# Optimization experiments

Measured on AMD Instinct MI355X. Metric: run time of the kernel, lower is better.

The kernel has to match this reference:

```python
import jax, jax.numpy as jnp
import numpy as np

NUM_CLASSES = 2
THRESH = 0.5        # overlap_thresh
NEGPOS = 3          # neg:pos ratio
VAR = (0.1, 0.2)    # cfg['variance']
B, P, O = 64, 32768, 50


def point_form(p):
    # center-size [cx,cy,w,h] -> corner [xmin,ymin,xmax,ymax]
    return jnp.concatenate([p[:, :2] - p[:, 2:] * 0.5, p[:, :2] + p[:, 2:] * 0.5], axis=1)


def iou(a, b):
    # a [O,4], b [P,4] corner form -> [O,P]
    lt = jnp.maximum(a[:, None, :2], b[None, :, :2])
    rb = jnp.minimum(a[:, None, 2:], b[None, :, 2:])
    wh = jnp.clip(rb - lt, 0.0, None)
    inter = wh[..., 0] * wh[..., 1]
    area_a = ((a[:, 2] - a[:, 0]) * (a[:, 3] - a[:, 1]))[:, None]
    area_b = ((b[:, 2] - b[:, 0]) * (b[:, 3] - b[:, 1]))[None, :]
    return inter / (area_a + area_b - inter)


def encode(matched, priors_cs):
    g_cxcy = ((matched[:, :2] + matched[:, 2:]) * 0.5 - priors_cs[:, :2]) / (VAR[0] * priors_cs[:, 2:])
    g_wh = jnp.log((matched[:, 2:] - matched[:, :2]) / priors_cs[:, 2:]) / VAR[1]
    return jnp.concatenate([g_cxcy, g_wh], axis=1)


def match_one(truths, labels, priors_cs, priors_pt):
    ovl = iou(truths, priors_pt)                # [O,P]
    best_prior_idx = jnp.argmax(ovl, axis=1)    # [O] best prior per GT
    best_truth_ovl = jnp.max(ovl, axis=0)       # [P]
    best_truth_idx = jnp.argmax(ovl, axis=0)    # [P]
    best_truth_ovl = best_truth_ovl.at[best_prior_idx].set(2.0)
    best_truth_idx = best_truth_idx.at[best_prior_idx].set(jnp.arange(truths.shape[0]))
    matched = truths[best_truth_idx]            # [P,4]
    conf = jnp.where(best_truth_ovl < THRESH, 0, labels[best_truth_idx])
    return encode(matched, priors_cs), conf


def reference(arm_loc, arm_conf, odm_loc, odm_conf, priors, targets):
    loc_data, conf_data = arm_loc, arm_conf    # use_ARM=False -> ARM branch
    num, num_priors = loc_data.shape[0], loc_data.shape[1]
    truths = targets[..., :4]
    labels = (targets[..., 4] >= 0).astype(jnp.int32)   # num_classes == 2 binarization
    priors_pt = point_form(priors)
    loc_t, conf_t = jax.vmap(lambda t, l: match_one(t, l, priors, priors_pt))(truths, labels)
    loc_t = jax.lax.stop_gradient(loc_t)
    conf_t = jax.lax.stop_gradient(conf_t)
    pos = conf_t > 0                             # [B,P]
    # localization: smooth L1, summed over positives
    d = loc_data - loc_t
    ad = jnp.abs(d)
    sl1 = jnp.where(ad < 1.0, 0.5 * d * d, ad - 0.5)
    loss_l = jnp.sum(sl1 * pos[..., None].astype(loc_data.dtype))
    # per-prior conf loss for hard negative mining
    lse = jax.nn.logsumexp(conf_data, axis=-1)   # [B,P]
    picked = jnp.take_along_axis(conf_data, conf_t[..., None], axis=-1)[..., 0]
    lc = lse - picked                            # NLL per prior
    lc_mine = jnp.where(pos, 0.0, lc)            # zero positives before ranking
    order = jnp.argsort(-lc_mine, axis=1)        # descending sort
    rank = jnp.argsort(order, axis=1)            # rank of each prior
    num_pos = jnp.sum(pos, axis=1, keepdims=True)            # [B,1]
    num_neg = jnp.minimum(NEGPOS * num_pos, num_priors - 1)
    neg = rank < num_neg
    sel = (pos | neg).astype(conf_data.dtype)
    loss_c = jnp.sum(lc * sel)
    N = jnp.sum(num_pos).astype(loc_data.dtype)
    return loss_l / N, loss_c / N


def setup_inputs():
    key = jax.random.key(0)
    ks = jax.random.split(key, 8)
    arm_loc = jax.random.normal(ks[0], (B, P, 4), jnp.float32)
    arm_conf = jax.random.normal(ks[1], (B, P, NUM_CLASSES), jnp.float32)
    odm_loc = jax.random.normal(ks[2], (B, P, 4), jnp.float32)
    odm_conf = jax.random.normal(ks[3], (B, P, NUM_CLASSES), jnp.float32)
    # priors in center-size form
    p_cxcy = jax.random.uniform(ks[4], (P, 2), jnp.float32, 0.05, 0.95)
    p_wh = jax.random.uniform(ks[5], (P, 2), jnp.float32, 0.05, 0.5)
    priors = jnp.concatenate([p_cxcy, p_wh], axis=1)
    # GT boxes in corner form with valid extents, labels >= 0
    t_cxcy = jax.random.uniform(ks[6], (B, O, 2), jnp.float32, 0.2, 0.8)
    t_wh = jax.random.uniform(ks[7], (B, O, 2), jnp.float32, 0.05, 0.3)
    boxes = jnp.concatenate([t_cxcy - t_wh * 0.5, t_cxcy + t_wh * 0.5], axis=-1)
    targets = jnp.concatenate([boxes, jnp.ones((B, O, 1), jnp.float32)], axis=-1)
    return {"arm_loc": arm_loc, "arm_conf": arm_conf, "odm_loc": odm_loc,
            "odm_conf": odm_conf, "priors": priors, "targets": targets}
```

## Files before the change

### kernel.cpp

```cpp
#include <hip/hip_runtime.h>
#include <cstdint>

#pragma clang fp contract(off)

#define BB 64
#define PP 32768
#define OO 50
#define THRESH_F 0.5f
#define VAR0 0.1f
#define VAR1 0.2f
#define NEGPOS_I 3
#define SS 32
#define T1 4
#define NB0 2048
#define NB12 1024

typedef unsigned long long u64;

__global__ void k_zero(float4* __restrict__ dst, int n4) {
    int i = blockIdx.x * blockDim.x + threadIdx.x;
    if (i < n4) dst[i] = make_float4(0.f, 0.f, 0.f, 0.f);
}

#define DPP_MAX(x, ctrl, rmask)                                              \
    {                                                                        \
        int _o = __float_as_int(x);                                          \
        x = fmaxf(x, __int_as_float(__builtin_amdgcn_update_dpp(             \
                _o, _o, (ctrl), (rmask), 0xf, false)));                      \
    }

__device__ __forceinline__ float sl1enc(const float* __restrict__ tb,
                                        float4 pr, float4 ld) {
    float gx = ((tb[0] + tb[2]) * 0.5f - pr.x) / (VAR0 * pr.z);
    float gy = ((tb[1] + tb[3]) * 0.5f - pr.y) / (VAR0 * pr.w);
    float gw = logf((tb[2] - tb[0]) / pr.z) / VAR1;
    float gh = logf((tb[3] - tb[1]) / pr.w) / VAR1;
    float g[4] = {gx, gy, gw, gh};
    float l[4] = {ld.x, ld.y, ld.z, ld.w};
    float s = 0.f;
    for (int q = 0; q < 4; ++q) {
        float d = l[q] - g[q];
        float ad = fabsf(d);
        s += (ad < 1.0f) ? 0.5f * d * d : ad - 0.5f;
    }
    return s;
}

__global__ void __launch_bounds__(256, 8)
k_ml(const float* __restrict__ priors, const float* __restrict__ targets,
     const float* __restrict__ arm_loc, const float* __restrict__ arm_conf,
     float* __restrict__ lcm, unsigned char* __restrict__ bpi,
     u64* __restrict__ bpm,
     float* __restrict__ pll, float* __restrict__ pplc, int* __restrict__ pnp,
     int* __restrict__ Hc0, float* __restrict__ Hs0) {
    __shared__ float tr4[OO * 4];
    __shared__ float trA[OO];
    __shared__ int   trL[OO];
    __shared__ int   hc[NB0];
    __shared__ float hs[NB0];
    int b = blockIdx.y, tid = threadIdx.x;
    for (int i = tid; i < OO * 4; i += 256)
        tr4[i] = targets[(size_t)(b * OO + (i >> 2)) * 5 + (i & 3)];
    if (tid < OO)
        trL[tid] = (targets[(size_t)(b * OO + tid) * 5 + 4] >= 0.0f) ? 1 : 0;
    for (int i = tid; i < NB0; i += 256) { hc[i] = 0; hs[i] = 0.f; }
    __syncthreads();
    if (tid < OO)
        trA[tid] = (tr4[tid*4+2] - tr4[tid*4]) * (tr4[tid*4+3] - tr4[tid*4+1]);
    __syncthreads();

    int p0 = blockIdx.x * (256 * T1) + tid * T1;
    float bx0[T1], by0[T1], bx1[T1], by1[T1], aB[T1];
#pragma unroll
    for (int j = 0; j < T1; ++j) {
        float4 pr = ((const float4*)priors)[p0 + j];
        bx0[j] = pr.x - pr.z * 0.5f; by0[j] = pr.y - pr.w * 0.5f;
        bx1[j] = pr.x + pr.z * 0.5f; by1[j] = pr.y + pr.w * 0.5f;
        aB[j] = (bx1[j] - bx0[j]) * (by1[j] - by0[j]);
    }
    float rbv[T1]; int rbi[T1];
#pragma unroll
    for (int j = 0; j < T1; ++j) { rbv[j] = -1.0f; rbi[j] = 0; }

    for (int t = 0; t < OO; ++t) {
        float t0 = tr4[t*4], t1v = tr4[t*4+1], t2 = tr4[t*4+2], t3 = tr4[t*4+3];
        float aA = trA[t];
        float cbv = -1.0f; int cbp = 0;
#pragma unroll
        for (int j = 0; j < T1; ++j) {
            float ltx = fmaxf(t0, bx0[j]), lty = fmaxf(t1v, by0[j]);
            float rbx = fminf(t2, bx1[j]), rby = fminf(t3, by1[j]);
            float wx = fmaxf(rbx - ltx, 0.f), wy = fmaxf(rby - lty, 0.f);
            float inter = wx * wy;
            float v = inter / (aA + aB[j] - inter);
            if (v > rbv[j]) { rbv[j] = v; rbi[j] = t; }
            if (v > cbv) { cbv = v; cbp = p0 + j; }
        }
        float x = cbv;
        DPP_MAX(x, 0x111, 0xf);
        DPP_MAX(x, 0x112, 0xf);
        DPP_MAX(x, 0x114, 0xf);
        DPP_MAX(x, 0x118, 0xf);
        DPP_MAX(x, 0x142, 0xa);
        DPP_MAX(x, 0x143, 0xc);
        float mv = __int_as_float(__builtin_amdgcn_readlane(__float_as_int(x), 63));
        unsigned long long msk = __ballot(cbv == mv);
        int lane = (int)__ffsll((long long)msk) - 1;
        int pwin = __builtin_amdgcn_readlane(cbp, lane);
        if ((tid & 63) == 0) {
            u64 pk = ((u64)__float_as_uint(mv) << 32) | (unsigned)(PP - pwin);
            atomicMax(&bpm[b * OO + t], pk);
        }
    }

    size_t bp = (size_t)b * PP + p0;
    float4 ca = ((const float4*)arm_conf)[bp >> 1];
    float4 cb = ((const float4*)arm_conf)[(bp >> 1) + 1];
    float cs[8] = {ca.x, ca.y, ca.z, ca.w, cb.x, cb.y, cb.z, cb.w};

    float ll = 0.0f, plc = 0.0f; int np = 0;
    float outv[4]; unsigned pbyte = 0;
#pragma unroll
    for (int c = 0; c < 4; ++c) {
        int ti = rbi[c]; float ov = rbv[c];
        int conf = (ov < THRESH_F) ? 0 : trL[ti];
        float c0 = cs[c*2], c1 = cs[c*2+1];
        float m = fmaxf(c0, c1);
        float lse = logf(expf(c0 - m) + expf(c1 - m)) + m;
        bool pos = conf > 0;
        float lc = lse - (pos ? c1 : c0);
        outv[c] = pos ? 0.0f : lc;
        pbyte |= (unsigned)((pos ? 0x80u : 0u) | (unsigned)ti) << (8 * c);
        unsigned u = __float_as_uint(outv[c]);
        atomicAdd(&hc[u >> 20], 1);
        atomicAdd(&hs[u >> 20], outv[c]);
        if (pos) {
            np++; plc += lc;
            float4 pr = ((const float4*)priors)[p0 + c];
            float4 ld = ((const float4*)arm_loc)[bp + c];
            ll += sl1enc(&tr4[ti * 4], pr, ld);
        }
    }
    ((float4*)lcm)[bp >> 2] = make_float4(outv[0], outv[1], outv[2], outv[3]);
    ((unsigned*)bpi)[bp >> 2] = pbyte;

    __syncthreads();
    for (int i = tid; i < NB0; i += 256) {
        int cv = hc[i];
        if (cv) {
            atomicAdd(&Hc0[b * NB0 + i], cv);
            atomicAdd(&Hs0[b * NB0 + i], hs[i]);
        }
    }
    __syncthreads();
    float* s1 = (float*)hc;
    int*   s3 = hc + 256;
    float* s2 = hs;
    s1[tid] = ll; s2[tid] = plc; s3[tid] = np;
    __syncthreads();
    for (int st = 128; st > 0; st >>= 1) {
        if (tid < st) { s1[tid] += s1[tid+st]; s2[tid] += s2[tid+st]; s3[tid] += s3[tid+st]; }
        __syncthreads();
    }
    if (tid == 0) {
        pll[blockIdx.x * BB + b] = s1[0];
        pplc[blockIdx.x * BB + b] = s2[0];
        pnp[blockIdx.x * BB + b] = s3[0];
    }
}

__global__ void k_fix(const u64* __restrict__ bpm, const float* __restrict__ targets,
                      const float* __restrict__ arm_loc, const float* __restrict__ arm_conf,
                      const float* __restrict__ priors, const unsigned char* __restrict__ bpi,
                      float* __restrict__ lcm,
                      float* __restrict__ pll, float* __restrict__ pplc,
                      int* __restrict__ pnp, int* __restrict__ npb,
                      int* __restrict__ Hc0, float* __restrict__ Hs0) {
    int b = blockIdx.x, j = threadIdx.x;
    int p = -1;
    if (j < OO) p = PP - (int)(unsigned)(bpm[b * OO + j] & 0xFFFFFFFFull);
    bool w = (j < OO);
    for (int jj = 1; jj < OO; ++jj) {
        int pj = __shfl(p, jj, 64);
        if (jj > j && pj == p) w = false;
    }
    float dll = 0.f, dplc = 0.f; int dnp = 0;
    if (w) {
        size_t bp = (size_t)b * PP + p;
        unsigned char ob = bpi[bp];
        bool old_pos = (ob & 0x80u) != 0;
        int old_ti = ob & 63;
        float2 cf = ((const float2*)arm_conf)[bp];
        float c0 = cf.x, c1 = cf.y;
        float m = fmaxf(c0, c1);
        float lse = logf(expf(c0 - m) + expf(c1 - m)) + m;
        const float* tbj = &targets[(size_t)(b * OO + j) * 5];
        bool new_pos = (tbj[4] >= 0.0f);
        float old_lcm = lcm[bp];
        float new_lcm = new_pos ? 0.0f : (lse - c0);
        unsigned uo = __float_as_uint(old_lcm), un = __float_as_uint(new_lcm);
        if (uo != un) {
            atomicAdd(&Hc0[b * NB0 + (uo >> 20)], -1);
            atomicAdd(&Hs0[b * NB0 + (uo >> 20)], -old_lcm);
            atomicAdd(&Hc0[b * NB0 + (un >> 20)], 1);
            atomicAdd(&Hs0[b * NB0 + (un >> 20)], new_lcm);
            lcm[bp] = new_lcm;
        }
        float4 pr = ((const float4*)priors)[p];
        float4 ld = ((const float4*)arm_loc)[bp];
        if (old_pos) {
            dnp -= 1; dplc -= (lse - c1);
            dll -= sl1enc(&targets[(size_t)(b * OO + old_ti) * 5], pr, ld);
        }
        if (new_pos) {
            dnp += 1; dplc += (lse - c1);
            dll += sl1enc(tbj, pr, ld);
        }
    }
    int myp = (j < SS) ? pnp[j * BB + b] : 0;
    for (int s = 32; s >= 1; s >>= 1) {
        dll += __shfl_down(dll, s, 64);
        dplc += __shfl_down(dplc, s, 64);
        dnp += __shfl_down(dnp, s, 64);
        myp += __shfl_down(myp, s, 64);
    }
    if (j == 0) {
        pll[b] += dll;
        pplc[b] += dplc;
        pnp[b] += dnp;
        npb[b] = myp + dnp;
    }
}

__global__ void __launch_bounds__(256)
k_sel(const float* __restrict__ lcm, const int* __restrict__ npb,
      int* __restrict__ Hc0, float* __restrict__ Hs0,
      float* __restrict__ ssum, int* __restrict__ srem, unsigned* __restrict__ stb) {
    __shared__ int hc[NB12]; __shared__ float hs[NB12];
    __shared__ int sc[256]; __shared__ float sf[256];
    __shared__ int s_chunk, s_r; __shared__ float s_S; __shared__ unsigned s_pref;
    int b = blockIdx.x, tid = threadIdx.x;

    {
        const int* hcg = Hc0 + b * NB0; const float* hsg = Hs0 + b * NB0;
        int c = 0; float f = 0.f; int base = tid * 8;
        for (int i = 0; i < 8; ++i) { c += hcg[base + i]; f += hsg[base + i]; }
        sc[tid] = c; sf[tid] = f;
        if (tid == 0) {
            int k = NEGPOS_I * npb[b]; if (k > PP - 1) k = PP - 1;
            s_r = k; s_S = 0.f;
        }
        __syncthreads();
        for (int off = 1; off < 256; off <<= 1) {
            int cv = (tid + off < 256) ? sc[tid + off] : 0;
            float fv = (tid + off < 256) ? sf[tid + off] : 0.f;
            __syncthreads(); sc[tid] += cv; sf[tid] += fv; __syncthreads();
        }
        int r = s_r;
        int nxt = (tid == 255) ? 0 : sc[tid + 1];
        if (sc[tid] >= r && nxt < r) s_chunk = tid;
        __syncthreads();
        if (tid == 0) {
            int ch = s_chunk;
            int r2 = r - ((ch == 255) ? 0 : sc[ch + 1]);
            float S2 = s_S + ((ch == 255) ? 0.f : sf[ch + 1]);
            int binSel = ch * 8;
            for (int i = 7; i >= 0; --i) {
                int bin = ch * 8 + i; int cbn = hcg[bin];
                if (r2 <= cbn) { binSel = bin; break; }
                r2 -= cbn; S2 += hsg[bin];
            }
            s_pref = (unsigned)binSel; s_r = r2; s_S = S2;
        }
        __syncthreads();
    }
    {
        for (int i = tid; i < NB12; i += 256) { hc[i] = 0; hs[i] = 0.f; }
        __syncthreads();
        unsigned pref = s_pref;
        const float4* v4 = (const float4*)(lcm + (size_t)b * PP);
        for (int it = 0; it < 32; ++it) {
            float4 x = v4[it * 256 + tid];
            float xs[4] = {x.x, x.y, x.z, x.w};
            for (int c2 = 0; c2 < 4; ++c2) {
                unsigned u = __float_as_uint(xs[c2]);
                if ((u >> 20) == pref) {
                    atomicAdd(&hc[(u >> 10) & 1023u], 1);
                    atomicAdd(&hs[(u >> 10) & 1023u], xs[c2]);
                }
            }
        }
        __syncthreads();
        int c = 0; float f = 0.f; int base = tid * 4;
        for (int i = 0; i < 4; ++i) { c += hc[base + i]; f += hs[base + i]; }
        sc[tid] = c; sf[tid] = f; __syncthreads();
        for (int off = 1; off < 256; off <<= 1) {
            int cv = (tid + off < 256) ? sc[tid + off] : 0;
            float fv = (tid + off < 256) ? sf[tid + off] : 0.f;
            __syncthreads(); sc[tid] += cv; sf[tid] += fv; __syncthreads();
        }
        int r = s_r;
        int nxt = (tid == 255) ? 0 : sc[tid + 1];
        if (sc[tid] >= r && nxt < r) s_chunk = tid;
        __syncthreads();
        if (tid == 0) {
            int ch = s_chunk;
            int r2 = r - ((ch == 255) ? 0 : sc[ch + 1]);
            float S2 = s_S + ((ch == 255) ? 0.f : sf[ch + 1]);
            int binSel = ch * 4;
            for (int i = 3; i >= 0; --i) {
                int bin = ch * 4 + i; int cbn = hc[bin];
                if (r2 <= cbn) { binSel = bin; break; }
                r2 -= cbn; S2 += hs[bin];
            }
            s_pref = (s_pref << 10) | (unsigned)binSel; s_r = r2; s_S = S2;
        }
        __syncthreads();
    }
    {
        for (int i = tid; i < NB12; i += 256) { hc[i] = 0; hs[i] = 0.f; }
        __syncthreads();
        unsigned pref = s_pref;
        const float4* v4 = (const float4*)(lcm + (size_t)b * PP);
        for (int it = 0; it < 32; ++it) {
            float4 x = v4[it * 256 + tid];
            float xs[4] = {x.x, x.y, x.z, x.w};
            for (int c2 = 0; c2 < 4; ++c2) {
                unsigned u = __float_as_uint(xs[c2]);
                if ((u >> 10) == pref) {
                    atomicAdd(&hc[u & 1023u], 1);
                    atomicAdd(&hs[u & 1023u], xs[c2]);
                }
            }
        }
        __syncthreads();
        int c = 0; float f = 0.f; int base = tid * 4;
        for (int i = 0; i < 4; ++i) { c += hc[base + i]; f += hs[base + i]; }
        sc[tid] = c; sf[tid] = f; __syncthreads();
        for (int off = 1; off < 256; off <<= 1) {
            int cv = (tid + off < 256) ? sc[tid + off] : 0;
            float fv = (tid + off < 256) ? sf[tid + off] : 0.f;
            __syncthreads(); sc[tid] += cv; sf[tid] += fv; __syncthreads();
        }
        int r = s_r;
        int nxt = (tid == 255) ? 0 : sc[tid + 1];
        if (sc[tid] >= r && nxt < r) s_chunk = tid;
        __syncthreads();
        if (tid == 0) {
            int ch = s_chunk;
            int r2 = r - ((ch == 255) ? 0 : sc[ch + 1]);
            float S2 = s_S + ((ch == 255) ? 0.f : sf[ch + 1]);
            int binSel = ch * 4;
            for (int i = 3; i >= 0; --i) {
                int bin = ch * 4 + i; int cbn = hc[bin];
                if (r2 <= cbn) { binSel = bin; break; }
                r2 -= cbn; S2 += hs[bin];
            }
            stb[b] = (s_pref << 10) | (unsigned)binSel;
            srem[b] = r2; ssum[b] = S2;
        }
    }
}

__global__ void k_final(const float* __restrict__ pll, const float* __restrict__ pplc,
                        const int* __restrict__ pnp, const float* __restrict__ ssum,
                        const int* __restrict__ srem, const unsigned* __restrict__ stb,
                        float* __restrict__ out) {
    int b = threadIdx.x;
    float ll = 0.f, plc = 0.f; int np = 0;
    for (int s = 0; s < SS; ++s) {
        ll += pll[s * BB + b];
        plc += pplc[s * BB + b];
        np += pnp[s * BB + b];
    }
    float tval = __uint_as_float(stb[b]);
    float cc = plc + ssum[b] + (float)srem[b] * tval;
    for (int s = 32; s > 0; s >>= 1) {
        ll += __shfl_down(ll, s);
        cc += __shfl_down(cc, s);
        np += __shfl_down(np, s);
    }
    if (b == 0) {
        float N = (float)np;
        out[0] = ll / N;
        out[1] = cc / N;
    }
}

extern "C" void kernel_launch(void* const* d_in, const int* in_sizes, int n_in,
                              void* d_out, int out_size, void* d_ws, size_t ws_size,
                              hipStream_t stream) {
    const float* arm_loc  = (const float*)d_in[0];
    const float* arm_conf = (const float*)d_in[1];
    const float* priors   = (const float*)d_in[4];
    const float* targets  = (const float*)d_in[5];
    float* out = (float*)d_out;

    char* w = (char*)d_ws;
    float* lcm = (float*)w;  w += sizeof(float) * (size_t)BB * PP;
    unsigned char* bpi = (unsigned char*)w; w += (size_t)BB * PP;
    char* zbase = w;
    int*   Hc0 = (int*)w;    w += sizeof(int)   * BB * NB0;
    float* Hs0 = (float*)w;  w += sizeof(float) * BB * NB0;
    u64*   bpm = (u64*)w;    w += sizeof(u64)   * BB * OO;
    size_t zbytes = (size_t)(w - zbase);
    float* pll  = (float*)w; w += sizeof(float) * BB * SS;
    float* pplc = (float*)w; w += sizeof(float) * BB * SS;
    int*   pnp  = (int*)w;   w += sizeof(int)   * BB * SS;
    int*   npb  = (int*)w;   w += sizeof(int)   * BB;
    unsigned* spre_unused = (unsigned*)w; w += sizeof(unsigned) * BB; (void)spre_unused;
    int*      srem = (int*)w;      w += sizeof(int) * BB;
    float*    ssum = (float*)w;    w += sizeof(float) * BB;
    unsigned* stb  = (unsigned*)w; w += sizeof(unsigned) * BB;

    int n4 = (int)(zbytes / 16);
    k_zero<<<(n4 + 255) / 256, 256, 0, stream>>>((float4*)zbase, n4);
    k_ml<<<dim3(SS, BB), 256, 0, stream>>>(priors, targets, arm_loc, arm_conf,
                                           lcm, bpi, bpm, pll, pplc, pnp, Hc0, Hs0);
    k_fix<<<BB, 64, 0, stream>>>(bpm, targets, arm_loc, arm_conf, priors, bpi,
                                 lcm, pll, pplc, pnp, npb, Hc0, Hs0);
    k_sel<<<BB, 256, 0, stream>>>(lcm, npb, Hc0, Hs0, ssum, srem, stb);
    k_final<<<1, 64, 0, stream>>>(pll, pplc, pnp, ssum, srem, stb, out);
}
```

Measured before the change: 267.1 us.

## Spatially sort priors into Morton cells and skip non-overlapping IoU wavefronts

Adds three small kernels that bin priors into a 16x16x4 Morton/size grid and build a permutation, so each wavefront of the matching kernel handles spatially clustered priors. When no lane in a wave has positive intersection with a GT box, the division, per-prior argmax update and wave reduction plus atomic are skipped. Ties are broken by original prior index with an integer DPP min, and the block-to-batch mapping is swizzled. In exchange, conf, loc and lcm/bpi accesses become gathers and scatters, and three extra launches are added.

```diff
diff --git a/kernel.cpp b/kernel.cpp
--- a/kernel.cpp
+++ b/kernel.cpp
@@ -14,12 +14,56 @@
 #define T1 4
 #define NB0 2048
 #define NB12 1024
+#define NCELL 1024
 
 typedef unsigned long long u64;
+
+__device__ __forceinline__ unsigned mpart4(unsigned x) {
+    x = (x | (x << 2)) & 0x33u;
+    x = (x | (x << 1)) & 0x55u;
+    return x;
+}
+__device__ __forceinline__ int cell_of(float4 pr) {
+    int xb = (int)(pr.x * 16.0f); xb = xb < 0 ? 0 : (xb > 15 ? 15 : xb);
+    int yb = (int)(pr.y * 16.0f); yb = yb < 0 ? 0 : (yb > 15 ? 15 : yb);
+    float s = fmaxf(pr.z, pr.w);
+    int wc = s < 0.275f ? 0 : (s < 0.368f ? 1 : (s < 0.44f ? 2 : 3));
+    return wc * 256 + (int)(mpart4((unsigned)xb) | (mpart4((unsigned)yb) << 1));
+}
 
 __global__ void k_zero(float4* __restrict__ dst, int n4) {
     int i = blockIdx.x * blockDim.x + threadIdx.x;
     if (i < n4) dst[i] = make_float4(0.f, 0.f, 0.f, 0.f);
+}
+
+__global__ void k_phist(const float4* __restrict__ pri, int* __restrict__ cnt) {
+    int p = blockIdx.x * 1024 + threadIdx.x * 4;
+    for (int j = 0; j < 4; ++j)
+        atomicAdd(&cnt[cell_of(pri[p + j])], 1);
+}
+
+__global__ void k_pscan(const int* __restrict__ cnt, int* __restrict__ base) {
+    __shared__ int sc[256];
+    int tid = threadIdx.x;
+    int a[4]; int s = 0;
+    for (int i = 0; i < 4; ++i) { a[i] = cnt[tid * 4 + i]; s += a[i]; }
+    sc[tid] = s; __syncthreads();
+    for (int off = 1; off < 256; off <<= 1) {
+        int v = (tid >= off) ? sc[tid - off] : 0;
+        __syncthreads(); sc[tid] += v; __syncthreads();
+    }
+    int excl = sc[tid] - s;
+    for (int i = 0; i < 4; ++i) { base[tid * 4 + i] = excl; excl += a[i]; }
+}
+
+__global__ void k_pscat(const float4* __restrict__ pri, const int* __restrict__ base,
+                        int* __restrict__ cursor, int* __restrict__ perm) {
+    int p = blockIdx.x * 1024 + threadIdx.x * 4;
+    for (int j = 0; j < 4; ++j) {
+        int c = cell_of(pri[p + j]);
+        int pos = base[c] + atomicAdd(&cursor[c], 1);
+        perm[pos] = p + j;
+    }
 }
 
 #define DPP_MAX(x, ctrl, rmask)                                              \
@@ -27,6 +71,12 @@
         int _o = __float_as_int(x);                                          \
         x = fmaxf(x, __int_as_float(__builtin_amdgcn_update_dpp(             \
                 _o, _o, (ctrl), (rmask), 0xf, false)));                      \
+    }
+#define DPP_MINI(x, ctrl, rmask)                                             \
+    {                                                                        \
+        int _o = (x);                                                        \
+        int _s = __builtin_amdgcn_update_dpp(_o, _o, (ctrl), (rmask), 0xf, false); \
+        x = (_s < x) ? _s : x;                                               \
     }
 
 __device__ __forceinline__ float sl1enc(const float* __restrict__ tb,
@@ -47,7 +97,8 @@
 }
 
 __global__ void __launch_bounds__(256, 8)
-k_ml(const float* __restrict__ priors, const float* __restrict__ targets,
+k_ml(const float* __restrict__ priors, const int* __restrict__ perm,
+     const float* __restrict__ targets,
      const float* __restrict__ arm_loc, const float* __restrict__ arm_conf,
      float* __restrict__ lcm, unsigned char* __restrict__ bpi,
      u64* __restrict__ bpm,
@@ -58,7 +109,9 @@
     __shared__ int   trL[OO];
     __shared__ int   hc[NB0];
     __shared__ float hs[NB0];
-    int b = blockIdx.y, tid = threadIdx.x;
+    int b = (blockIdx.x % 8) * 8 + (blockIdx.y % 8);
+    int s = (blockIdx.x / 8) + 4 * (blockIdx.y / 8);
+    int tid = threadIdx.x;
     for (int i = tid; i < OO * 4; i += 256)
         tr4[i] = targets[(size_t)(b * OO + (i >> 2)) * 5 + (i & 3)];
     if (tid < OO)
@@ -69,80 +122,93 @@
         trA[tid] = (tr4[tid*4+2] - tr4[tid*4]) * (tr4[tid*4+3] - tr4[tid*4+1]);
     __syncthreads();
 
-    int p0 = blockIdx.x * (256 * T1) + tid * T1;
+    int p0 = s * (256 * T1) + tid * T1;
+    int4 o4 = ((const int4*)perm)[p0 >> 2];
+    int o_[T1] = {o4.x, o4.y, o4.z, o4.w};
+    int omin = min(min(o_[0], o_[1]), min(o_[2], o_[3]));
     float bx0[T1], by0[T1], bx1[T1], by1[T1], aB[T1];
 #pragma unroll
     for (int j = 0; j < T1; ++j) {
-        float4 pr = ((const float4*)priors)[p0 + j];
+        float4 pr = ((const float4*)priors)[o_[j]];
         bx0[j] = pr.x - pr.z * 0.5f; by0[j] = pr.y - pr.w * 0.5f;
         bx1[j] = pr.x + pr.z * 0.5f; by1[j] = pr.y + pr.w * 0.5f;
         aB[j] = (bx1[j] - bx0[j]) * (by1[j] - by0[j]);
     }
     float rbv[T1]; int rbi[T1];
 #pragma unroll
-    for (int j = 0; j < T1; ++j) { rbv[j] = -1.0f; rbi[j] = 0; }
+    for (int j = 0; j < T1; ++j) { rbv[j] = 0.0f; rbi[j] = 0; }
 
     for (int t = 0; t < OO; ++t) {
         float t0 = tr4[t*4], t1v = tr4[t*4+1], t2 = tr4[t*4+2], t3 = tr4[t*4+3];
         float aA = trA[t];
-        float cbv = -1.0f; int cbp = 0;
+        float I[T1];
 #pragma unroll
         for (int j = 0; j < T1; ++j) {
             float ltx = fmaxf(t0, bx0[j]), lty = fmaxf(t1v, by0[j]);
             float rbx = fminf(t2, bx1[j]), rby = fminf(t3, by1[j]);
             float wx = fmaxf(rbx - ltx, 0.f), wy = fmaxf(rby - lty, 0.f);
-            float inter = wx * wy;
-            float v = inter / (aA + aB[j] - inter);
-            if (v > rbv[j]) { rbv[j] = v; rbi[j] = t; }
-            if (v > cbv) { cbv = v; cbp = p0 + j; }
-        }
-        float x = cbv;
-        DPP_MAX(x, 0x111, 0xf);
-        DPP_MAX(x, 0x112, 0xf);
-        DPP_MAX(x, 0x114, 0xf);
-        DPP_MAX(x, 0x118, 0xf);
-        DPP_MAX(x, 0x142, 0xa);
-        DPP_MAX(x, 0x143, 0xc);
-        float mv = __int_as_float(__builtin_amdgcn_readlane(__float_as_int(x), 63));
-        unsigned long long msk = __ballot(cbv == mv);
-        int lane = (int)__ffsll((long long)msk) - 1;
-        int pwin = __builtin_amdgcn_readlane(cbp, lane);
-        if ((tid & 63) == 0) {
-            u64 pk = ((u64)__float_as_uint(mv) << 32) | (unsigned)(PP - pwin);
-            atomicMax(&bpm[b * OO + t], pk);
-        }
-    }
-
-    size_t bp = (size_t)b * PP + p0;
-    float4 ca = ((const float4*)arm_conf)[bp >> 1];
-    float4 cb = ((const float4*)arm_conf)[(bp >> 1) + 1];
-    float cs[8] = {ca.x, ca.y, ca.z, ca.w, cb.x, cb.y, cb.z, cb.w};
-
+            I[j] = wx * wy;
+        }
+        bool anyl = (I[0] > 0.f) | (I[1] > 0.f) | (I[2] > 0.f) | (I[3] > 0.f);
+        if (__any(anyl)) {
+            float cbv = 0.0f; int cbo = omin;
+#pragma unroll
+            for (int j = 0; j < T1; ++j) {
+                float v = I[j] / (aA + aB[j] - I[j]);
+                if (v > rbv[j]) { rbv[j] = v; rbi[j] = t; }
+                if (v > cbv || (v == cbv && o_[j] < cbo)) { cbv = v; cbo = o_[j]; }
+            }
+            float x = cbv;
+            DPP_MAX(x, 0x111, 0xf);
+            DPP_MAX(x, 0x112, 0xf);
+            DPP_MAX(x, 0x114, 0xf);
+            DPP_MAX(x, 0x118, 0xf);
+            DPP_MAX(x, 0x142, 0xa);
+            DPP_MAX(x, 0x143, 0xc);
+            float mvf = __int_as_float(__builtin_amdgcn_readlane(__float_as_int(x), 63));
+            if (mvf > 0.0f) {
+                int key = (cbv == mvf) ? cbo : 0x7FFFFFFF;
+                DPP_MINI(key, 0x111, 0xf);
+                DPP_MINI(key, 0x112, 0xf);
+                DPP_MINI(key, 0x114, 0xf);
+                DPP_MINI(key, 0x118, 0xf);
+                DPP_MINI(key, 0x142, 0xa);
+                DPP_MINI(key, 0x143, 0xc);
+                int morig = __builtin_amdgcn_readlane(key, 63);
+                if ((tid & 63) == 0) {
+                    u64 pk = ((u64)__float_as_uint(mvf) << 32) | (unsigned)(PP - morig);
+                    atomicMax(&bpm[b * OO + t], pk);
+                }
+            }
+        }
+    }
+
+    size_t bbase = (size_t)b * PP;
     float ll = 0.0f, plc = 0.0f; int np = 0;
-    float outv[4]; unsigned pbyte = 0;
 #pragma unroll
-    for (int c = 0; c < 4; ++c) {
+    for (int c = 0; c < T1; ++c) {
+        int o = o_[c]; size_t bo = bbase + o;
         int ti = rbi[c]; float ov = rbv[c];
         int conf = (ov < THRESH_F) ? 0 : trL[ti];
-        float c0 = cs[c*2], c1 = cs[c*2+1];
+        float2 cf = ((const float2*)arm_conf)[bo];
+        float c0 = cf.x, c1 = cf.y;
         float m = fmaxf(c0, c1);
         float lse = logf(expf(c0 - m) + expf(c1 - m)) + m;
         bool pos = conf > 0;
         float lc = lse - (pos ? c1 : c0);
-        outv[c] = pos ? 0.0f : lc;
-        pbyte |= (unsigned)((pos ? 0x80u : 0u) | (unsigned)ti) << (8 * c);
-        unsigned u = __float_as_uint(outv[c]);
+        float outv = pos ? 0.0f : lc;
+        lcm[bo] = outv;
+        bpi[bo] = (unsigned char)((pos ? 0x80u : 0u) | (unsigned)ti);
+        unsigned u = __float_as_uint(outv);
         atomicAdd(&hc[u >> 20], 1);
-        atomicAdd(&hs[u >> 20], outv[c]);
+        atomicAdd(&hs[u >> 20], outv);
         if (pos) {
             np++; plc += lc;
-            float4 pr = ((const float4*)priors)[p0 + c];
-            float4 ld = ((const float4*)arm_loc)[bp + c];
+            float4 pr = ((const float4*)priors)[o];
+            float4 ld = ((const float4*)arm_loc)[bo];
             ll += sl1enc(&tr4[ti * 4], pr, ld);
         }
     }
-    ((float4*)lcm)[bp >> 2] = make_float4(outv[0], outv[1], outv[2], outv[3]);
-    ((unsigned*)bpi)[bp >> 2] = pbyte;
 
     __syncthreads();
     for (int i = tid; i < NB0; i += 256) {
@@ -163,9 +229,9 @@
         __syncthreads();
     }
     if (tid == 0) {
-        pll[blockIdx.x * BB + b] = s1[0];
-        pplc[blockIdx.x * BB + b] = s2[0];
-        pnp[blockIdx.x * BB + b] = s3[0];
+        pll[s * BB + b] = s1[0];
+        pplc[s * BB + b] = s2[0];
+        pnp[s * BB + b] = s3[0];
     }
 }
 
@@ -178,7 +244,10 @@
                       int* __restrict__ Hc0, float* __restrict__ Hs0) {
     int b = blockIdx.x, j = threadIdx.x;
     int p = -1;
-    if (j < OO) p = PP - (int)(unsigned)(bpm[b * OO + j] & 0xFFFFFFFFull);
+    if (j < OO) {
+        unsigned lo = (unsigned)(bpm[b * OO + j] & 0xFFFFFFFFull);
+        p = lo ? (PP - (int)lo) : 0;
+    }
     bool w = (j < OO);
     for (int jj = 1; jj < OO; ++jj) {
         int pj = __shfl(p, jj, 64);
@@ -403,19 +472,25 @@
     int*   Hc0 = (int*)w;    w += sizeof(int)   * BB * NB0;
     float* Hs0 = (float*)w;  w += sizeof(float) * BB * NB0;
     u64*   bpm = (u64*)w;    w += sizeof(u64)   * BB * OO;
+    int*   cellCnt = (int*)w; w += sizeof(int) * NCELL;
+    int*   cursor  = (int*)w; w += sizeof(int) * NCELL;
     size_t zbytes = (size_t)(w - zbase);
+    int*   cellBase = (int*)w; w += sizeof(int) * NCELL;
+    int*   perm = (int*)w;   w += sizeof(int) * PP;
     float* pll  = (float*)w; w += sizeof(float) * BB * SS;
     float* pplc = (float*)w; w += sizeof(float) * BB * SS;
     int*   pnp  = (int*)w;   w += sizeof(int)   * BB * SS;
     int*   npb  = (int*)w;   w += sizeof(int)   * BB;
-    unsigned* spre_unused = (unsigned*)w; w += sizeof(unsigned) * BB; (void)spre_unused;
     int*      srem = (int*)w;      w += sizeof(int) * BB;
     float*    ssum = (float*)w;    w += sizeof(float) * BB;
     unsigned* stb  = (unsigned*)w; w += sizeof(unsigned) * BB;
 
     int n4 = (int)(zbytes / 16);
     k_zero<<<(n4 + 255) / 256, 256, 0, stream>>>((float4*)zbase, n4);
-    k_ml<<<dim3(SS, BB), 256, 0, stream>>>(priors, targets, arm_loc, arm_conf,
+    k_phist<<<PP / 1024, 256, 0, stream>>>((const float4*)priors, cellCnt);
+    k_pscan<<<1, 256, 0, stream>>>(cellCnt, cellBase);
+    k_pscat<<<PP / 1024, 256, 0, stream>>>((const float4*)priors, cellBase, cursor, perm);
+    k_ml<<<dim3(SS, BB), 256, 0, stream>>>(priors, perm, targets, arm_loc, arm_conf,
                                            lcm, bpi, bpm, pll, pplc, pnp, Hc0, Hs0);
     k_fix<<<BB, 64, 0, stream>>>(bpm, targets, arm_loc, arm_conf, priors, bpi,
                                  lcm, pll, pplc, pnp, npb, Hc0, Hs0);
```

Result: slower. 280.5 us (+5.0%).
